# Kernel tuning notes

Measured on AMD Instinct MI355X. Metric: run time of the kernel, lower is better.

The kernel has to match this reference:

```python
import jax, jax.numpy as jnp
import numpy as np


def setup_inputs() -> dict:
    key = jax.random.key(0)
    ks = jax.random.split(key, 8)
    B, C, H, W = 16, 256, 64, 64
    E, heads, R = 256, 8, 64
    s = 0.02  # small init scale in lieu of xavier
    return {
        "x": jax.random.normal(ks[0], (B, C, H, W), dtype=jnp.float32),
        "Wqkv": jax.random.normal(ks[1], (3 * E, C), dtype=jnp.float32) * s,
        "bqkv": jnp.zeros((3 * E,), dtype=jnp.float32),
        "Wr": jax.random.normal(ks[2], (2 * R * heads, C), dtype=jnp.float32) * s,
        "br": jnp.zeros((2 * R * heads,), dtype=jnp.float32),
        "Wout": jax.random.normal(ks[3], (C, E), dtype=jnp.float32) * s,
        "bout": jnp.zeros((C,), dtype=jnp.float32),
        "alpha": jax.random.normal(ks[4], (1,), dtype=jnp.float32),
        "num_heads": heads,
        "num_regions": R,
    }


def reference(x, Wqkv, bqkv, Wr, br, Wout, bout, alpha, num_heads, num_regions):
    B, C, H, W = x.shape
    N = H * W
    E = Wqkv.shape[0] // 3
    d = E // num_heads  # head_dim
    xf = x.reshape(B, C, N)  # [B, C, N]

    # qkv 1x1 conv -> [B, 3E, N] -> [B, h, N, 3d] -> q,k,v [B, h, N, d]
    qkv = jnp.einsum("oc,bcn->bon", Wqkv, xf) + bqkv[:, None]
    qkv = qkv.reshape(B, num_heads, 3 * d, N).transpose(0, 1, 3, 2)
    q, k, v = jnp.split(qkv, 3, axis=-1)

    # region projections: 1x1 conv + softmax over the FULL channel axis (2*R*heads)
    r = jnp.einsum("oc,bcn->bon", Wr, xf) + br[:, None]
    r = jax.nn.softmax(r, axis=1)
    r = r.reshape(B, num_heads, 2 * num_regions, N).transpose(0, 1, 3, 2)
    Rq, Rk = jnp.split(r, 2, axis=-1)  # each [B, h, N, R]

    # pool tokens into regions: [B, h, d, R]
    qr = jnp.einsum("bhnd,bhnr->bhdr", q, Rq)
    kr = jnp.einsum("bhnd,bhnr->bhdr", k, Rk)
    vr = jnp.einsum("bhnd,bhnr->bhdr", v, Rk)

    # region-level attention [B, h, Rq, Rk], scaled by sqrt(head_dim)
    logits = jnp.einsum("bhdq,bhdk->bhqk", qr, kr) / jnp.sqrt(jnp.asarray(d, x.dtype))
    attn = jax.nn.softmax(logits, axis=-1)  # dropout is identity at eval

    # values = v_r @ attn^T -> [B, h, d, Rq]; expand back to tokens via Rq^T
    vals = jnp.einsum("bhdk,bhqk->bhdq", vr, attn)
    vals = jnp.einsum("bhdq,bhnq->bhdn", vals, Rq)  # [B, h, d, N]

    vals = vals.reshape(B, E, N)
    out = jnp.einsum("oe,ben->bon", Wout, vals) + bout[:, None]
    out = out.reshape(B, C, H, W)
    return x + alpha * out
```

## Files before the change

kernel.cpp:

```cpp
#include <hip/hip_runtime.h>
#include <cstdint>

typedef unsigned short ushort_t;
typedef __attribute__((ext_vector_type(4))) unsigned short ushort4_t;
typedef __attribute__((ext_vector_type(8))) unsigned short ushort8_t;
typedef __attribute__((ext_vector_type(8))) __bf16 bf16x8;
typedef __attribute__((ext_vector_type(4))) float f32x4;

constexpr int NB = 16;
constexpr int NC = 256;
constexpr int NN = 4096;
constexpr int NP = 1024;
constexpr int NT = 512;
constexpr int NO = 768;

static __device__ __forceinline__ ushort_t f2b(float f) {
  uint32_t u = __builtin_bit_cast(uint32_t, f);
  u += 0x7FFFu + ((u >> 16) & 1u);
  return (ushort_t)(u >> 16);
}
static __device__ __forceinline__ float b2f(ushort_t h) {
  return __builtin_bit_cast(float, (uint32_t)h << 16);
}
static __device__ __forceinline__ f32x4 mfma16(bf16x8 a, bf16x8 b, f32x4 c) {
  return __builtin_amdgcn_mfma_f32_16x16x32_bf16(a, b, c, 0, 0, 0);
}
typedef __attribute__((address_space(1))) const unsigned int guint;
typedef __attribute__((address_space(3))) unsigned int luint;
static __device__ __forceinline__ void glds16(const void* g, void* l) {
  __builtin_amdgcn_global_load_lds((guint*)g, (luint*)l, 16, 0, 0);
}

template <int KITERS>
__device__ __forceinline__ void gemm_core_sb(const ushort_t* __restrict__ Asrc, size_t lda,
                                             const ushort_t* __restrict__ Bsrc, size_t ldb,
                                             ushort_t* SH, f32x4 (&acc)[4][4], int tid) {
  const int l = tid & 63, w = tid >> 6;
  const int fr = l & 15, kq = (l >> 4) * 8;
  const int rr = l >> 3;
  const int sc = ((l & 7) ^ rr) << 3;
  const int swz = (fr & 7) << 3;
  const int wm = (w >> 1) * 64, wn = (w & 1) * 64;
  ushort_t* As = SH;
  ushort_t* Bs = SH + 8192;
#pragma unroll 1
  for (int it = 0; it < KITERS; it++) {
    const size_t k0 = (size_t)it * 64;
#pragma unroll
    for (int i = 0; i < 4; i++) {
      const int row = i * 32 + w * 8 + rr;
      glds16(Asrc + (size_t)row * lda + k0 + sc, As + (i * 32 + w * 8) * 64);
      glds16(Bsrc + (size_t)row * ldb + k0 + sc, Bs + (i * 32 + w * 8) * 64);
    }
    __syncthreads();
#pragma unroll
    for (int ks = 0; ks < 2; ks++) {
      const int col = ks * 32 + kq;
      bf16x8 af[4], bf[4];
#pragma unroll
      for (int f = 0; f < 4; f++) {
        af[f] = *(const bf16x8*)&As[(wm + f * 16 + fr) * 64 + (col ^ swz)];
        bf[f] = *(const bf16x8*)&Bs[(wn + f * 16 + fr) * 64 + (col ^ swz)];
      }
#pragma unroll
      for (int fm = 0; fm < 4; fm++)
#pragma unroll
        for (int fn = 0; fn < 4; fn++)
          acc[fm][fn] = mfma16(af[fm], bf[fn], acc[fm][fn]);
    }
    __syncthreads();
  }
}

__global__ __launch_bounds__(256) void k0_cvt(const float* __restrict__ x,
                                              ushort_t* __restrict__ xb,
                                              ushort_t* __restrict__ xt) {
  __shared__ ushort_t tr[64][88];
  const int tid = threadIdx.x;
  const int n0 = blockIdx.x * 64, c0 = blockIdx.y * 64, b = blockIdx.z;
  const int cr = (tid >> 4) * 4;
  const int nc4 = (tid & 15) * 4;
#pragma unroll
  for (int i = 0; i < 4; i++) {
    size_t idx = ((size_t)b * NC + c0 + cr + i) * NN + n0 + nc4;
    float4 v = *(const float4*)(x + idx);
    ushort4_t o;
    o[0] = f2b(v.x); o[1] = f2b(v.y); o[2] = f2b(v.z); o[3] = f2b(v.w);
    *(ushort4_t*)(xb + idx) = o;
    tr[nc4 + 0][cr + i] = o[0];
    tr[nc4 + 1][cr + i] = o[1];
    tr[nc4 + 2][cr + i] = o[2];
    tr[nc4 + 3][cr + i] = o[3];
  }
  __syncthreads();
  const int nr = tid >> 2, cc0 = (tid & 3) * 16;
  size_t odx = ((size_t)b * NN + n0 + nr) * NC + c0 + cc0;
  *(ushort8_t*)(xt + odx) = *(const ushort8_t*)&tr[nr][cc0];
  *(ushort8_t*)(xt + odx + 8) = *(const ushort8_t*)&tr[nr][cc0 + 8];
}

__global__ __launch_bounds__(256) void cvt_f2b_k(const float* __restrict__ src,
                                                 ushort_t* __restrict__ dst) {
  int i = (blockIdx.x * 256 + threadIdx.x) * 4;
  float4 v = *(const float4*)(src + i);
  ushort4_t o;
  o[0] = f2b(v.x); o[1] = f2b(v.y); o[2] = f2b(v.z); o[3] = f2b(v.w);
  *(ushort4_t*)(dst + i) = o;
}

__global__ __launch_bounds__(256) void k1_proj(const ushort_t* __restrict__ Wrb,
                                               const ushort_t* __restrict__ xt,
                                               const float* __restrict__ br,
                                               ushort_t* __restrict__ P) {
  __shared__ __align__(16) ushort_t SH[16384];
  const int tid = threadIdx.x;
  const int ord = blockIdx.x;
  const int L = (ord & 7) * 512 + (ord >> 3);
  const int m0 = (L & 7) * 128;
  const int n0 = ((L >> 3) & 31) * 128;
  const int b = L >> 8;
  const int lane = tid & 63, w = tid >> 6;
  const int wm = (w >> 1) * 64, wn = (w & 1) * 64;
  f32x4 acc[4][4] = {};
  gemm_core_sb<4>(Wrb + (size_t)m0 * NC, NC,
                  xt + ((size_t)b * NN + n0) * NC, NC, SH, acc, tid);
  const int col = lane & 15, rb = (lane >> 4) * 4;
#pragma unroll
  for (int fm = 0; fm < 4; fm++)
#pragma unroll
    for (int rg = 0; rg < 4; rg++) {
      int row = m0 + wm + fm * 16 + rb + rg;
      float bias = br[row];
#pragma unroll
      for (int fn = 0; fn < 4; fn++) {
        int cc = n0 + wn + fn * 16 + col;
        P[((size_t)b * NP + row) * NN + cc] = f2b(acc[fm][fn][rg] + bias);
      }
    }
}

__global__ __launch_bounds__(512) void k2_softmax(ushort_t* __restrict__ P,
                                                  float* __restrict__ sPpart) {
  __shared__ float red[64][64];
  __shared__ float Mf[64], If[64];
  const int tid = threadIdx.x;
  const int n0 = blockIdx.x * 64, b = blockIdx.y;
  const int cg = tid & 7, pg = tid >> 3;
  ushort_t* base = P + (size_t)b * NP * NN + n0 + cg * 8;

  ushort8_t v[16];
  float m[8];
#pragma unroll
  for (int j = 0; j < 8; j++) m[j] = -3.0e38f;
#pragma unroll
  for (int r = 0; r < 16; r++) {
    v[r] = *(const ushort8_t*)(base + (size_t)(pg * 16 + r) * NN);
#pragma unroll
    for (int j = 0; j < 8; j++) m[j] = fmaxf(m[j], b2f(v[r][j]));
  }
#pragma unroll
  for (int j = 0; j < 8; j++) red[pg][cg * 8 + j] = m[j];
  __syncthreads();
  if (tid < 64) {
    float M = -3.0e38f;
    for (int g = 0; g < 64; g++) M = fmaxf(M, red[g][tid]);
    Mf[tid] = M;
  }
  __syncthreads();
  float mj[8], s[8];
#pragma unroll
  for (int j = 0; j < 8; j++) { mj[j] = Mf[cg * 8 + j]; s[j] = 0.f; }
#pragma unroll
  for (int r = 0; r < 16; r++)
#pragma unroll
    for (int j = 0; j < 8; j++) s[j] += __expf(b2f(v[r][j]) - mj[j]);
#pragma unroll
  for (int j = 0; j < 8; j++) red[pg][cg * 8 + j] = s[j];
  __syncthreads();
  if (tid < 64) {
    float S = 0.f;
    for (int g = 0; g < 64; g++) S += red[g][tid];
    If[tid] = 1.f / S;
  }
  __syncthreads();
  float ij[8];
#pragma unroll
  for (int j = 0; j < 8; j++) ij[j] = If[cg * 8 + j];
#pragma unroll
  for (int r = 0; r < 16; r++) {
    int p = pg * 16 + r;
    ushort8_t o;
    float rs = 0.f;
#pragma unroll
    for (int j = 0; j < 8; j++) {
      float e = __expf(b2f(v[r][j]) - mj[j]) * ij[j];
      o[j] = f2b(e);
      rs += e;
    }
    *(ushort8_t*)(base + (size_t)p * NN) = o;
    rs += __shfl_xor(rs, 1, 64);
    rs += __shfl_xor(rs, 2, 64);
    rs += __shfl_xor(rs, 4, 64);
    if (cg == 0) sPpart[((size_t)blockIdx.x * NB + b) * NP + p] = rs;
  }
}

__global__ __launch_bounds__(256) void k2r_reduce(const float* __restrict__ sPpart,
                                                  float* __restrict__ sP) {
  int idx = blockIdx.x * 256 + threadIdx.x;
  float s = 0.f;
#pragma unroll 8
  for (int bx = 0; bx < 64; bx++) s += sPpart[(size_t)bx * (NB * NP) + idx];
  sP[idx] = s;
}

__global__ __launch_bounds__(256) void k3_pool(const ushort_t* __restrict__ xb,
                                               const ushort_t* __restrict__ P,
                                               ushort_t* __restrict__ XRbT) {
  __shared__ __align__(16) ushort_t SH[4 * 8192];
  const int tid = threadIdx.x;
  const int ord = blockIdx.x;
  const int L = (ord & 7) * 32 + (ord >> 3);
  const int m0 = (L & 1) * 128;
  const int n0 = ((L >> 1) & 7) * 128;
  const int b = L >> 4;
  const int l = tid & 63, w = tid >> 6;
  const int fr = l & 15, kq = (l >> 4) * 8;
  const int rr = l >> 3;
  const int sc = ((l & 7) ^ rr) << 3;
  const int swz = (fr & 7) << 3;
  const int wm = (w >> 1) * 64, wn = (w & 1) * 64;
  const ushort_t* Asrc = xb + ((size_t)b * NC + m0) * NN;
  const ushort_t* Bsrc = P + ((size_t)b * NP + n0) * NN;
  f32x4 acc[4][4] = {};

  auto STAGE = [&](int bi, size_t k0) {
    ushort_t* Ad = SH + bi * 8192;
    ushort_t* Bd = SH + 16384 + bi * 8192;
#pragma unroll
    for (int i = 0; i < 4; i++) {
      const int row = i * 32 + w * 8 + rr;
      glds16(Asrc + (size_t)row * NN + k0 + sc, Ad + (i * 32 + w * 8) * 64);
      glds16(Bsrc + (size_t)row * NN + k0 + sc, Bd + (i * 32 + w * 8) * 64);
    }
  };

  STAGE(0, 0);
  __syncthreads();
  int cur = 0;
#pragma unroll 1
  for (int it = 0; it < 64; it++) {
    if (it + 1 < 64) STAGE(cur ^ 1, (size_t)(it + 1) * 64);
    const ushort_t* Ar = SH + cur * 8192;
    const ushort_t* Br = SH + 16384 + cur * 8192;
#pragma unroll
    for (int ks = 0; ks < 2; ks++) {
      const int col = ks * 32 + kq;
      bf16x8 af[4], bf[4];
#pragma unroll
      for (int f = 0; f < 4; f++) {
        af[f] = *(const bf16x8*)&Ar[(wm + f * 16 + fr) * 64 + (col ^ swz)];
        bf[f] = *(const bf16x8*)&Br[(wn + f * 16 + fr) * 64 + (col ^ swz)];
      }
#pragma unroll
      for (int fm = 0; fm < 4; fm++)
#pragma unroll
        for (int fn = 0; fn < 4; fn++)
          acc[fm][fn] = mfma16(af[fm], bf[fn], acc[fm][fn]);
    }
    __syncthreads();
    cur ^= 1;
  }
  const int colc = l & 15, rb = (l >> 4) * 4;
#pragma unroll
  for (int pp = 0; pp < 2; pp++) {
    if ((w & 1) == pp) {
#pragma unroll
      for (int fm = 0; fm < 4; fm++)
#pragma unroll
        for (int rg = 0; rg < 4; rg++) {
          const int cl = wm + fm * 16 + rb + rg;
#pragma unroll
          for (int fn = 0; fn < 4; fn++) {
            const int pl = fn * 16 + colc;
            SH[pl * 136 + cl] = f2b(acc[fm][fn][rg]);
          }
        }
    }
    __syncthreads();
    const int prow = tid >> 2, cch = (tid & 3) * 32;
    ushort_t* dst = XRbT + ((size_t)b * NP + n0 + pp * 64 + prow) * NC + m0 + cch;
    const ushort_t* s = &SH[prow * 136 + cch];
#pragma unroll
    for (int j = 0; j < 4; j++)
      *(ushort8_t*)(dst + j * 8) = *(const ushort8_t*)(s + j * 8);
    __syncthreads();
  }
}

__global__ __launch_bounds__(256) void k4a_qkvr(const ushort_t* __restrict__ Wqkvb,
                                                const ushort_t* __restrict__ XRbT,
                                                const float* __restrict__ bqkv,
                                                const float* __restrict__ sP,
                                                ushort_t* __restrict__ QKVRb) {
  __shared__ __align__(16) ushort_t SH[2 * 8192];
  const int tid = threadIdx.x;
  const int ord = blockIdx.x;
  const int L = (ord & 7) * 96 + (ord >> 3);
  const int m0 = (L % 6) * 128;
  const int rest = L / 6;
  const int n0 = (rest & 7) * 128;
  const int b = rest >> 3;
  const int lane = tid & 63, w = tid >> 6;
  const int wm = (w >> 1) * 64, wn = (w & 1) * 64;
  f32x4 acc[4][4] = {};
  gemm_core_sb<4>(Wqkvb + (size_t)m0 * NC, NC,
                  XRbT + ((size_t)b * NP + n0) * NC, NC, SH, acc, tid);
  const int col = lane & 15, rb = (lane >> 4) * 4;
  float spv[4];
#pragma unroll
  for (int fn = 0; fn < 4; fn++) spv[fn] = sP[(size_t)b * NP + n0 + wn + fn * 16 + col];
#pragma unroll
  for (int fm = 0; fm < 4; fm++)
#pragma unroll
    for (int rg = 0; rg < 4; rg++) {
      int row = m0 + wm + fm * 16 + rb + rg;
      float bq = bqkv[row];
#pragma unroll
      for (int fn = 0; fn < 4; fn++) {
        int cc = n0 + wn + fn * 16 + col;
        QKVRb[((size_t)b * NO + row) * NP + cc] = f2b(acc[fm][fn][rg] + bq * spv[fn]);
      }
    }
}

__global__ __launch_bounds__(256) void k4b_attn(const ushort_t* __restrict__ QKVRb,
                                                const float* __restrict__ Wout,
                                                ushort_t* __restrict__ Tmb) {
  const int b = blockIdx.x >> 3, h = blockIdx.x & 7;
  const int tid = threadIdx.x;
  __shared__ float qf[96][64];
  __shared__ float attn_sT[64][65];
  __shared__ float vals_s[32][64];
#pragma unroll
  for (int i = 0; i < 3; i++) {
    int u = i * 256 + tid;
    int rw = u >> 3, jc = (u & 7) * 8;
    int p0 = h * 128 + ((rw < 32) ? 0 : 64);
    ushort8_t v = *(const ushort8_t*)(QKVRb + ((size_t)b * NO + h * 96 + rw) * NP + p0 + jc);
#pragma unroll
    for (int j = 0; j < 8; j++) qf[rw][jc + j] = b2f(v[j]);
  }
  __syncthreads();
  const int lj = tid & 63;
  const int rq = tid >> 6;
  float kcol[32];
#pragma unroll
  for (int dd = 0; dd < 32; dd++) kcol[dd] = qf[32 + dd][lj];
  const float isc = 0.17677669529663687f;
#pragma unroll
  for (int r = 0; r < 16; r++) {
    int qi = r * 4 + rq;
    float a = 0.f;
#pragma unroll
    for (int dd = 0; dd < 32; dd++) a += qf[dd][qi] * kcol[dd];
    attn_sT[lj][qi] = a * isc;
  }
  __syncthreads();
  if (tid < 64) {
    float m = -3e38f;
    for (int k = 0; k < 64; k++) m = fmaxf(m, attn_sT[k][tid]);
    float s = 0.f;
    for (int k = 0; k < 64; k++) {
      float e = __expf(attn_sT[k][tid] - m);
      attn_sT[k][tid] = e;
      s += e;
    }
    float inv = 1.f / s;
    for (int k = 0; k < 64; k++) attn_sT[k][tid] *= inv;
  }
  __syncthreads();
  float acol[64];
#pragma unroll
  for (int k = 0; k < 64; k++) acol[k] = attn_sT[k][lj];
#pragma unroll
  for (int r = 0; r < 8; r++) {
    int dd = r * 4 + rq;
    float a = 0.f;
#pragma unroll
    for (int k = 0; k < 64; k++) a += qf[64 + dd][k] * acol[k];
    vals_s[dd][lj] = a;
  }
  __syncthreads();
  float vcol[32];
#pragma unroll
  for (int dd = 0; dd < 32; dd++) vcol[dd] = vals_s[dd][lj];
  for (int r = 0; r < 64; r++) {
    int c = r * 4 + rq;
    const float4* wp = (const float4*)(Wout + (size_t)c * NC + h * 32);
    float a = 0.f;
#pragma unroll
    for (int t = 0; t < 8; t++) {
      float4 w = wp[t];
      a += w.x * vcol[t * 4] + w.y * vcol[t * 4 + 1] + w.z * vcol[t * 4 + 2] +
           w.w * vcol[t * 4 + 3];
    }
    Tmb[((size_t)b * NC + c) * NT + h * 64 + lj] = f2b(a);
  }
}

__global__ __launch_bounds__(256) void k5_out(const float* __restrict__ x,
                                              const ushort_t* __restrict__ P,
                                              const ushort_t* __restrict__ Tmb,
                                              const float* __restrict__ bout,
                                              const float* __restrict__ alpha,
                                              float* __restrict__ out) {
  __shared__ __align__(16) ushort_t Ash[2 * 8192];
  __shared__ __align__(16) ushort_t Bsh[2 * 9216];
  const int tid = threadIdx.x;
  const int ord = blockIdx.x;
  const int L = (ord & 7) * 128 + (ord >> 3);
  const int m0 = (L & 1) * 128;
  const int n0 = ((L >> 1) & 31) * 128;
  const int b = L >> 6;
  const int lane = tid & 63, w = tid >> 6;
  const int wm = (w >> 1) * 64, wn = (w & 1) * 64;
  const int fr = lane & 15, kq = (lane >> 4) * 8;
  const int rr = lane >> 3, sc = ((lane & 7) ^ rr) << 3;
  const int swz = (fr & 7) << 3;
  const ushort_t* Asrc = Tmb + ((size_t)b * NC + m0) * NT;
  const int kg = tid >> 5, ng = (tid & 31) * 4;
  f32x4 acc[4][4] = {};
  ushort4_t bv[8];

  auto A_STAGE = [&](int bi, int k0) {
    ushort_t* Ad = Ash + bi * 8192;
#pragma unroll
    for (int i = 0; i < 4; i++) {
      const int row = i * 32 + w * 8 + rr;
      glds16(Asrc + (size_t)row * NT + k0 + sc, Ad + (i * 32 + w * 8) * 64);
    }
  };
  auto B_LOAD = [&](int k0) {
#pragma unroll
    for (int i = 0; i < 8; i++) {
      int hj = k0 + kg * 8 + i;
      int prow = ((hj >> 6) << 7) + (hj & 63);
      bv[i] = *(const ushort4_t*)(P + ((size_t)b * NP + prow) * NN + n0 + ng);
    }
  };
  auto B_WRITE = [&](int bi) {
#pragma unroll
    for (int jj = 0; jj < 4; jj++) {
      ushort8_t pk;
#pragma unroll
      for (int i = 0; i < 8; i++) pk[i] = bv[i][jj];
      *(ushort8_t*)&Bsh[bi * 9216 + (ng + jj) * 72 + kg * 8] = pk;
    }
  };

  A_STAGE(0, 0);
  B_LOAD(0);
  B_WRITE(0);
  __syncthreads();
  int cur = 0;
#pragma unroll 1
  for (int it = 0; it < 8; it++) {
    if (it + 1 < 8) {
      A_STAGE(cur ^ 1, (it + 1) * 64);
      B_LOAD((it + 1) * 64);
    }
    const ushort_t* Ar = Ash + cur * 8192;
    const ushort_t* Br = Bsh + cur * 9216;
#pragma unroll
    for (int ks = 0; ks < 2; ks++) {
      const int col = ks * 32 + kq;
      bf16x8 af[4], bf[4];
#pragma unroll
      for (int f = 0; f < 4; f++) {
        af[f] = *(const bf16x8*)&Ar[(wm + f * 16 + fr) * 64 + (col ^ swz)];
        bf[f] = *(const bf16x8*)&Br[(wn + f * 16 + fr) * 72 + col];
      }
#pragma unroll
      for (int fm = 0; fm < 4; fm++)
#pragma unroll
        for (int fn = 0; fn < 4; fn++)
          acc[fm][fn] = mfma16(af[fm], bf[fn], acc[fm][fn]);
    }
    if (it + 1 < 8) B_WRITE(cur ^ 1);
    __syncthreads();
    cur ^= 1;
  }
  const float al = alpha[0];
  const int col = lane & 15, rb = (lane >> 4) * 4;
#pragma unroll
  for (int fm = 0; fm < 4; fm++)
#pragma unroll
    for (int rg = 0; rg < 4; rg++) {
      int row = m0 + wm + fm * 16 + rb + rg;
      float bias = bout[row];
#pragma unroll
      for (int fn = 0; fn < 4; fn++) {
        int cc = n0 + wn + fn * 16 + col;
        size_t idx = ((size_t)b * NC + row) * NN + cc;
        out[idx] = x[idx] + al * (acc[fm][fn][rg] + bias);
      }
    }
}

extern "C" void kernel_launch(void* const* d_in, const int* in_sizes, int n_in,
                              void* d_out, int out_size, void* d_ws, size_t ws_size,
                              hipStream_t stream) {
  const float* x = (const float*)d_in[0];
  const float* Wqkv = (const float*)d_in[1];
  const float* bqkv = (const float*)d_in[2];
  const float* Wr = (const float*)d_in[3];
  const float* br = (const float*)d_in[4];
  const float* Wout = (const float*)d_in[5];
  const float* bout = (const float*)d_in[6];
  const float* alpha = (const float*)d_in[7];
  float* out = (float*)d_out;

  char* ws = (char*)d_ws;
  ushort_t* P = (ushort_t*)ws;
  ushort_t* xb = (ushort_t*)(ws + 134217728);
  ushort_t* QKVRb = (ushort_t*)(ws + 134217728);
  ushort_t* xt = (ushort_t*)(ws + 167772160);
  ushort_t* XRbT = (ushort_t*)(ws + 167772160);
  ushort_t* Wrb = (ushort_t*)(ws + 201326592);
  float* sPpart = (float*)(ws + 201850880);
  ushort_t* Wqkvb = (ushort_t*)(ws + 201850880);
  float* sP = (float*)(ws + 206045184);
  ushort_t* Tmb = (ushort_t*)(ws + 206110720);

  k0_cvt<<<dim3(64, 4, 16), 256, 0, stream>>>(x, xb, xt);
  cvt_f2b_k<<<256, 256, 0, stream>>>(Wr, Wrb);
  k1_proj<<<4096, 256, 0, stream>>>(Wrb, xt, br, P);
  k2_softmax<<<dim3(64, 16), 512, 0, stream>>>(P, sPpart);
  k2r_reduce<<<64, 256, 0, stream>>>(sPpart, sP);
  cvt_f2b_k<<<192, 256, 0, stream>>>(Wqkv, Wqkvb);
  k3_pool<<<256, 256, 0, stream>>>(xb, P, XRbT);
  k4a_qkvr<<<768, 256, 0, stream>>>(Wqkvb, XRbT, bqkv, sP, QKVRb);
  k4b_attn<<<128, 256, 0, stream>>>(QKVRb, Wout, Tmb);
  k5_out<<<1024, 256, 0, stream>>>(x, P, Tmb, bout, alpha, out);
}
```

Measured before the change: 334.1 us.

## Fuse QKV region projection into attention kernel and single-buffer k5 B tile

The separate k4a QKV GEMM over region-pooled features is merged into the per-(batch,head) attention kernel. Each block now computes only the 96x128 slice it needs with MFMA from swizzled LDS and keeps the result in shared memory, which drops the QKVRb global round trip and one launch. The fused kernel uses about 112KB of LDS and only 128 blocks, so the GEMM runs with low parallelism. Separately, k5_out's B tile goes from double to single buffering, which adds an extra barrier per iteration but lowers LDS use so more blocks may fit per CU.

```diff
diff --git a/kernel.cpp b/kernel.cpp
--- a/kernel.cpp
+++ b/kernel.cpp
@@ -298,112 +298,143 @@
   }
 }
 
-__global__ __launch_bounds__(256) void k4a_qkvr(const ushort_t* __restrict__ Wqkvb,
+__global__ __launch_bounds__(256) void k4f_attn(const ushort_t* __restrict__ Wqkvb,
                                                 const ushort_t* __restrict__ XRbT,
                                                 const float* __restrict__ bqkv,
                                                 const float* __restrict__ sP,
-                                                ushort_t* __restrict__ QKVRb) {
-  __shared__ __align__(16) ushort_t SH[2 * 8192];
-  const int tid = threadIdx.x;
-  const int ord = blockIdx.x;
-  const int L = (ord & 7) * 96 + (ord >> 3);
-  const int m0 = (L % 6) * 128;
-  const int rest = L / 6;
-  const int n0 = (rest & 7) * 128;
-  const int b = rest >> 3;
-  const int lane = tid & 63, w = tid >> 6;
-  const int wm = (w >> 1) * 64, wn = (w & 1) * 64;
-  f32x4 acc[4][4] = {};
-  gemm_core_sb<4>(Wqkvb + (size_t)m0 * NC, NC,
-                  XRbT + ((size_t)b * NP + n0) * NC, NC, SH, acc, tid);
-  const int col = lane & 15, rb = (lane >> 4) * 4;
-  float spv[4];
-#pragma unroll
-  for (int fn = 0; fn < 4; fn++) spv[fn] = sP[(size_t)b * NP + n0 + wn + fn * 16 + col];
-#pragma unroll
-  for (int fm = 0; fm < 4; fm++)
-#pragma unroll
-    for (int rg = 0; rg < 4; rg++) {
-      int row = m0 + wm + fm * 16 + rb + rg;
-      float bq = bqkv[row];
-#pragma unroll
-      for (int fn = 0; fn < 4; fn++) {
-        int cc = n0 + wn + fn * 16 + col;
-        QKVRb[((size_t)b * NO + row) * NP + cc] = f2b(acc[fm][fn][rg] + bq * spv[fn]);
-      }
-    }
-}
-
-__global__ __launch_bounds__(256) void k4b_attn(const ushort_t* __restrict__ QKVRb,
                                                 const float* __restrict__ Wout,
                                                 ushort_t* __restrict__ Tmb) {
+  __shared__ __align__(16) char SHRAW[114688];
+  ushort_t* Aw = (ushort_t*)SHRAW;
+  ushort_t* Bw = (ushort_t*)(SHRAW + 49152);
+  float* qf = (float*)SHRAW;
+  float* attn_sT = (float*)(SHRAW + 24576);
+  float* vals_s = (float*)(SHRAW + 41216);
   const int b = blockIdx.x >> 3, h = blockIdx.x & 7;
   const int tid = threadIdx.x;
-  __shared__ float qf[96][64];
-  __shared__ float attn_sT[64][65];
-  __shared__ float vals_s[32][64];
-#pragma unroll
-  for (int i = 0; i < 3; i++) {
-    int u = i * 256 + tid;
-    int rw = u >> 3, jc = (u & 7) * 8;
-    int p0 = h * 128 + ((rw < 32) ? 0 : 64);
-    ushort8_t v = *(const ushort8_t*)(QKVRb + ((size_t)b * NO + h * 96 + rw) * NP + p0 + jc);
-#pragma unroll
-    for (int j = 0; j < 8; j++) qf[rw][jc + j] = b2f(v[j]);
+  const int l = tid & 63, w = tid >> 6;
+  const ushort_t* Asrc = Wqkvb + (size_t)(h * 96) * NC;
+  const ushort_t* Bsrc = XRbT + ((size_t)b * NP + h * 128) * NC;
+  {
+    const int r2 = l >> 5;
+    const int oct = l & 31;
+#pragma unroll
+    for (int i = 0; i < 12; i++) {
+      const int rbase = (i * 4 + w) * 2;
+      const int row = rbase + r2;
+      const int scol = (oct ^ (row & 7)) * 8;
+      glds16(Asrc + (size_t)row * NC + scol, Aw + rbase * 256);
+    }
+#pragma unroll
+    for (int i = 0; i < 16; i++) {
+      const int rbase = (i * 4 + w) * 2;
+      const int row = rbase + r2;
+      const int scol = (oct ^ (row & 7)) * 8;
+      glds16(Bsrc + (size_t)row * NC + scol, Bw + rbase * 256);
+    }
+  }
+  __syncthreads();
+  const int fr = l & 15, kq = (l >> 4) * 8;
+  const int swz = (fr & 7) << 3;
+  f32x4 acc[6][2] = {};
+#pragma unroll
+  for (int ks = 0; ks < 8; ks++) {
+    const int col = ks * 32 + kq;
+    bf16x8 bf[2];
+#pragma unroll
+    for (int f = 0; f < 2; f++)
+      bf[f] = *(const bf16x8*)&Bw[(w * 32 + f * 16 + fr) * 256 + (col ^ swz)];
+#pragma unroll
+    for (int fm = 0; fm < 6; fm++) {
+      bf16x8 af = *(const bf16x8*)&Aw[(fm * 16 + fr) * 256 + (col ^ swz)];
+#pragma unroll
+      for (int f = 0; f < 2; f++) acc[fm][f] = mfma16(af, bf[f], acc[fm][f]);
+    }
+  }
+  __syncthreads();
+  {
+    const int rb = (l >> 4) * 4;
+    float spv[2];
+#pragma unroll
+    for (int f = 0; f < 2; f++)
+      spv[f] = sP[(size_t)b * NP + h * 128 + w * 32 + f * 16 + fr];
+    if (w < 2) {
+#pragma unroll
+      for (int fm = 0; fm < 2; fm++)
+#pragma unroll
+        for (int rg = 0; rg < 4; rg++) {
+          const int row = fm * 16 + rb + rg;
+          const float bq = bqkv[h * 96 + row];
+#pragma unroll
+          for (int f = 0; f < 2; f++)
+            qf[row * 64 + w * 32 + f * 16 + fr] = acc[fm][f][rg] + bq * spv[f];
+        }
+    } else {
+#pragma unroll
+      for (int fm = 2; fm < 6; fm++)
+#pragma unroll
+        for (int rg = 0; rg < 4; rg++) {
+          const int row = fm * 16 + rb + rg;
+          const float bq = bqkv[h * 96 + row];
+#pragma unroll
+          for (int f = 0; f < 2; f++)
+            qf[row * 64 + (w - 2) * 32 + f * 16 + fr] = acc[fm][f][rg] + bq * spv[f];
+        }
+    }
   }
   __syncthreads();
   const int lj = tid & 63;
   const int rq = tid >> 6;
   float kcol[32];
 #pragma unroll
-  for (int dd = 0; dd < 32; dd++) kcol[dd] = qf[32 + dd][lj];
+  for (int dd = 0; dd < 32; dd++) kcol[dd] = qf[(32 + dd) * 64 + lj];
   const float isc = 0.17677669529663687f;
 #pragma unroll
   for (int r = 0; r < 16; r++) {
     int qi = r * 4 + rq;
     float a = 0.f;
 #pragma unroll
-    for (int dd = 0; dd < 32; dd++) a += qf[dd][qi] * kcol[dd];
-    attn_sT[lj][qi] = a * isc;
+    for (int dd = 0; dd < 32; dd++) a += qf[dd * 64 + qi] * kcol[dd];
+    attn_sT[lj * 65 + qi] = a * isc;
   }
   __syncthreads();
   if (tid < 64) {
     float m = -3e38f;
-    for (int k = 0; k < 64; k++) m = fmaxf(m, attn_sT[k][tid]);
+    for (int k = 0; k < 64; k++) m = fmaxf(m, attn_sT[k * 65 + tid]);
     float s = 0.f;
     for (int k = 0; k < 64; k++) {
-      float e = __expf(attn_sT[k][tid] - m);
-      attn_sT[k][tid] = e;
+      float e = __expf(attn_sT[k * 65 + tid] - m);
+      attn_sT[k * 65 + tid] = e;
       s += e;
     }
     float inv = 1.f / s;
-    for (int k = 0; k < 64; k++) attn_sT[k][tid] *= inv;
+    for (int k = 0; k < 64; k++) attn_sT[k * 65 + tid] *= inv;
   }
   __syncthreads();
   float acol[64];
 #pragma unroll
-  for (int k = 0; k < 64; k++) acol[k] = attn_sT[k][lj];
+  for (int k = 0; k < 64; k++) acol[k] = attn_sT[k * 65 + lj];
 #pragma unroll
   for (int r = 0; r < 8; r++) {
     int dd = r * 4 + rq;
     float a = 0.f;
 #pragma unroll
-    for (int k = 0; k < 64; k++) a += qf[64 + dd][k] * acol[k];
-    vals_s[dd][lj] = a;
+    for (int k = 0; k < 64; k++) a += qf[(64 + dd) * 64 + k] * acol[k];
+    vals_s[dd * 64 + lj] = a;
   }
   __syncthreads();
   float vcol[32];
 #pragma unroll
-  for (int dd = 0; dd < 32; dd++) vcol[dd] = vals_s[dd][lj];
+  for (int dd = 0; dd < 32; dd++) vcol[dd] = vals_s[dd * 64 + lj];
   for (int r = 0; r < 64; r++) {
     int c = r * 4 + rq;
     const float4* wp = (const float4*)(Wout + (size_t)c * NC + h * 32);
     float a = 0.f;
 #pragma unroll
     for (int t = 0; t < 8; t++) {
-      float4 w = wp[t];
-      a += w.x * vcol[t * 4] + w.y * vcol[t * 4 + 1] + w.z * vcol[t * 4 + 2] +
-           w.w * vcol[t * 4 + 3];
+      float4 ww = wp[t];
+      a += ww.x * vcol[t * 4] + ww.y * vcol[t * 4 + 1] + ww.z * vcol[t * 4 + 2] +
+           ww.w * vcol[t * 4 + 3];
     }
     Tmb[((size_t)b * NC + c) * NT + h * 64 + lj] = f2b(a);
   }
@@ -416,7 +447,7 @@
                                               const float* __restrict__ alpha,
                                               float* __restrict__ out) {
   __shared__ __align__(16) ushort_t Ash[2 * 8192];
-  __shared__ __align__(16) ushort_t Bsh[2 * 9216];
+  __shared__ __align__(16) ushort_t Bsh[128 * 72];
   const int tid = threadIdx.x;
   const int ord = blockIdx.x;
   const int L = (ord & 7) * 128 + (ord >> 3);
@@ -449,29 +480,28 @@
       bv[i] = *(const ushort4_t*)(P + ((size_t)b * NP + prow) * NN + n0 + ng);
     }
   };
-  auto B_WRITE = [&](int bi) {
+  auto B_WRITE = [&]() {
 #pragma unroll
     for (int jj = 0; jj < 4; jj++) {
       ushort8_t pk;
 #pragma unroll
       for (int i = 0; i < 8; i++) pk[i] = bv[i][jj];
-      *(ushort8_t*)&Bsh[bi * 9216 + (ng + jj) * 72 + kg * 8] = pk;
+      *(ushort8_t*)&Bsh[(ng + jj) * 72 + kg * 8] = pk;
     }
   };
 
+  B_LOAD(0);
   A_STAGE(0, 0);
-  B_LOAD(0);
-  B_WRITE(0);
-  __syncthreads();
-  int cur = 0;
+  B_WRITE();
+  __syncthreads();
+  int acur = 0;
 #pragma unroll 1
   for (int it = 0; it < 8; it++) {
-    if (it + 1 < 8) {
-      A_STAGE(cur ^ 1, (it + 1) * 64);
+    if (it < 7) {
       B_LOAD((it + 1) * 64);
-    }
-    const ushort_t* Ar = Ash + cur * 8192;
-    const ushort_t* Br = Bsh + cur * 9216;
+      A_STAGE(acur ^ 1, (it + 1) * 64);
+    }
+    const ushort_t* Ar = Ash + acur * 8192;
 #pragma unroll
     for (int ks = 0; ks < 2; ks++) {
       const int col = ks * 32 + kq;
@@ -479,7 +509,7 @@
 #pragma unroll
       for (int f = 0; f < 4; f++) {
         af[f] = *(const bf16x8*)&Ar[(wm + f * 16 + fr) * 64 + (col ^ swz)];
-        bf[f] = *(const bf16x8*)&Br[(wn + f * 16 + fr) * 72 + col];
+        bf[f] = *(const bf16x8*)&Bsh[(wn + f * 16 + fr) * 72 + col];
       }
 #pragma unroll
       for (int fm = 0; fm < 4; fm++)
@@ -487,9 +517,12 @@
         for (int fn = 0; fn < 4; fn++)
           acc[fm][fn] = mfma16(af[fm], bf[fn], acc[fm][fn]);
     }
-    if (it + 1 < 8) B_WRITE(cur ^ 1);
     __syncthreads();
-    cur ^= 1;
+    if (it < 7) {
+      B_WRITE();
+      __syncthreads();
+    }
+    acur ^= 1;
   }
   const float al = alpha[0];
   const int col = lane & 15, rb = (lane >> 4) * 4;
@@ -524,7 +557,6 @@
   char* ws = (char*)d_ws;
   ushort_t* P = (ushort_t*)ws;
   ushort_t* xb = (ushort_t*)(ws + 134217728);
-  ushort_t* QKVRb = (ushort_t*)(ws + 134217728);
   ushort_t* xt = (ushort_t*)(ws + 167772160);
   ushort_t* XRbT = (ushort_t*)(ws + 167772160);
   ushort_t* Wrb = (ushort_t*)(ws + 201326592);
@@ -540,7 +572,6 @@
   k2r_reduce<<<64, 256, 0, stream>>>(sPpart, sP);
   cvt_f2b_k<<<192, 256, 0, stream>>>(Wqkv, Wqkvb);
   k3_pool<<<256, 256, 0, stream>>>(xb, P, XRbT);
-  k4a_qkvr<<<768, 256, 0, stream>>>(Wqkvb, XRbT, bqkv, sP, QKVRb);
-  k4b_attn<<<128, 256, 0, stream>>>(QKVRb, Wout, Tmb);
+  k4f_attn<<<128, 256, 0, stream>>>(Wqkvb, XRbT, bqkv, sP, Wout, Tmb);
   k5_out<<<1024, 256, 0, stream>>>(x, P, Tmb, bout, alpha, out);
 }
```

Result: no change. 329.4 us (-1.4%).
